# Kernel tuning notes

Measured on AMD Instinct MI355X. Metric: run time of the kernel, lower is better.

The kernel has to match this reference:

```python
import jax, jax.numpy as jnp
import numpy as np
import math

N_NODES = 50000
N_EDGES = 800000
IN_DIM = 128
OUT_DIM = 64
TIME_DIM = 128


def setup_inputs() -> dict:
    key = jax.random.key(0)
    ks = jax.random.split(key, 9)
    return {
        "node_feats": jax.random.normal(ks[0], (N_NODES, IN_DIM), dtype=jnp.float32),
        "time_diff": jax.random.uniform(ks[1], (N_EDGES,), dtype=jnp.float32),
        "src": jax.random.randint(ks[2], (N_EDGES,), 0, N_NODES, dtype=jnp.int32),
        "dst": jax.random.randint(ks[3], (N_EDGES,), 0, N_NODES, dtype=jnp.int32),
        "W": jax.random.normal(ks[4], (OUT_DIM, IN_DIM), dtype=jnp.float32) * 0.05,
        "Wv": jax.random.normal(ks[5], (OUT_DIM, IN_DIM), dtype=jnp.float32) * 0.05,
        "omega": jax.random.normal(ks[6], (TIME_DIM // 2,), dtype=jnp.float32),
        "Wt": jax.random.normal(ks[7], (OUT_DIM, TIME_DIM), dtype=jnp.float32) * 0.05,
        "a": jax.random.normal(ks[8], (3 * OUT_DIM,), dtype=jnp.float32) * 0.05,
    }


def reference(node_feats, time_diff, src, dst, W, Wv, omega, Wt, a):
    N = node_feats.shape[0]
    d = W.shape[0]  # out_dim
    time_dim = 2 * omega.shape[0]

    # gather + linear projections per edge
    h_src = node_feats[src] @ W.T          # [E, d]
    h_dst = node_feats[dst] @ W.T          # [E, d]
    v_src = node_feats[src] @ Wv.T         # [E, d]

    # temporal encoding: interleaved sin/cos of t * omega, scaled by sqrt(1/dim)
    ang = time_diff[:, None] * omega[None, :]                       # [E, dim/2]
    pe = jnp.stack([jnp.sin(ang), jnp.cos(ang)], axis=-1)
    pe = pe.reshape(ang.shape[0], time_dim) * jnp.float32(math.sqrt(1.0 / time_dim))
    t_emb = pe @ Wt.T                                               # [E, d]

    # attn_fc(concat([h_src, h_dst, t_emb])) == split dot products (same math, no big concat)
    e = h_src @ a[:d] + h_dst @ a[d:2 * d] + t_emb @ a[2 * d:]      # [E]
    e = jnp.where(e > 0, e, 0.2 * e)  # LeakyReLU(0.2)

    # edge_softmax: softmax over incoming edges of each destination node
    m = jax.ops.segment_max(e, dst, num_segments=N)
    ex = jnp.exp(e - m[dst])
    den = jax.ops.segment_sum(ex, dst, num_segments=N)
    alpha = ex / den[dst]  # dropout is identity in eval mode

    # weighted message scatter-sum aggregation
    msg = v_src * alpha[:, None]                                    # [E, d]
    return jax.ops.segment_sum(msg, dst, num_segments=N)            # [N, d]
```

## Files before the change

kernel.cpp:

```cpp
#include <hip/hip_runtime.h>
#include <hip/hip_bf16.h>
#include <hip/hip_fp16.h>
#include <math.h>

#define IN_DIM   128
#define OUT_DIM  64
#define THALF    64
#define PE_SCALE 0.08838834764831845f
#define TBL      2048
#define EPB_LOG  14
#define EPB      (1 << EPB_LOG)

typedef __attribute__((ext_vector_type(8))) short  short8;
typedef __attribute__((ext_vector_type(4))) float  f32x4;

__device__ inline unsigned short bf16_rne(float x) {
    unsigned u = __float_as_uint(x);
    return (unsigned short)((u + 0x7FFFu + ((u >> 16) & 1u)) >> 16);
}

__global__ __launch_bounds__(256) void k_prep(
    const float* __restrict__ W, const float* __restrict__ Wt,
    const float* __restrict__ a, const float* __restrict__ Wv,
    const float* __restrict__ omega,
    float* __restrict__ gtab, unsigned short* __restrict__ Bp,
    int* __restrict__ pref)
{
    __shared__ float satv[IN_DIM];
    __shared__ float saW1[IN_DIM], saW2[IN_DIM];
    int t = threadIdx.x;
    if (t < IN_DIM) {
        float x3 = 0.f;
        for (int j = 0; j < OUT_DIM; ++j)
            x3 += a[2 * OUT_DIM + j] * Wt[j * IN_DIM + t];
        satv[t] = x3;
        if (blockIdx.x == 0) {
            float x1 = 0.f, x2 = 0.f;
            for (int j = 0; j < OUT_DIM; ++j) {
                float wj = W[j * IN_DIM + t];
                x1 += a[j] * wj;
                x2 += a[OUT_DIM + j] * wj;
            }
            saW1[t] = x1; saW2[t] = x2;
        }
    }
    __syncthreads();

    int idx = blockIdx.x * 256 + t;
    if (idx <= TBL) {
        float tt = (float)idx * (1.0f / TBL);
        float acc = 0.f;
#pragma unroll
        for (int i = 0; i < THALF; ++i) {
            float sp, cp;
            __sincosf(tt * omega[i], &sp, &cp);
            acc += sp * satv[2 * i] + cp * satv[2 * i + 1];
        }
        gtab[idx] = acc;
    }
    if (idx < 64) pref[idx] = 0;

    if (blockIdx.x == 0) {
        for (int i = t; i < 5 * 4 * 64 * 8; i += 256) {
            int j    = i & 7;
            int lane = (i >> 3) & 63;
            int k0i  = (i >> 9) & 3;
            int tt   = i >> 11;
            int kk = k0i * 32 + (lane >> 4) * 8 + j;
            int n  = lane & 15;
            float val;
            if (tt < 4)     val = Wv[(tt * 16 + n) * IN_DIM + kk];
            else            val = (n == 0) ? saW1[kk] : (n == 1) ? saW2[kk] : 0.f;
            Bp[i] = bf16_rne(val);
        }
    }
}

__global__ __launch_bounds__(1024) void k_hist(
    const int* __restrict__ dst,
    unsigned short* __restrict__ lrank,
    unsigned* __restrict__ ghist,
    int N, int E)
{
    extern __shared__ unsigned h[];
    int NH = (N + 1) >> 1;
    int t = threadIdx.x;
    for (int i = t; i < NH; i += 1024) h[i] = 0u;
    __syncthreads();
    int b = blockIdx.x;
    int e0 = b << EPB_LOG;
    int e1 = e0 + EPB; if (e1 > E) e1 = E;
    for (int e = e0 + t; e < e1; e += 1024) {
        int d = dst[e];
        unsigned inc = (d & 1) ? 0x10000u : 1u;
        unsigned old = atomicAdd(&h[d >> 1], inc);
        lrank[e] = (unsigned short)((d & 1) ? (old >> 16) : (old & 0xFFFFu));
    }
    __syncthreads();
    unsigned* gh = ghist + (size_t)b * N;
    for (int w = t; w < NH; w += 1024) {
        unsigned v = h[w];
        int n0 = 2 * w;
        if (n0 + 1 < N) *(uint2*)(gh + n0) = make_uint2(v & 0xFFFFu, v >> 16);
        else            gh[n0] = v & 0xFFFFu;
    }
}

__global__ __launch_bounds__(256) void k_scan_base(
    unsigned* __restrict__ ghist, int* __restrict__ cnt, int B, int N)
{
    int n0 = (blockIdx.x * 256 + threadIdx.x) * 2;
    if (n0 >= N) return;
    if (n0 + 1 < N) {
        unsigned r0 = 0, r1 = 0;
        for (int b = 0; b < B; ++b) {
            unsigned* p = ghist + (size_t)b * N + n0;
            uint2 c = *(uint2*)p;
            *(uint2*)p = make_uint2(r0, r1);
            r0 += c.x; r1 += c.y;
        }
        *(int2*)(cnt + n0) = make_int2((int)r0, (int)r1);
    } else {
        unsigned r0 = 0;
        for (int b = 0; b < B; ++b) {
            unsigned* p = ghist + (size_t)b * N + n0;
            unsigned c = *p; *p = r0; r0 += c;
        }
        cnt[n0] = (int)r0;
    }
}

__global__ __launch_bounds__(256) void k_scan1(const int* __restrict__ cnt,
                                               int* __restrict__ offs,
                                               int* __restrict__ pref, int N)
{
    __shared__ int lds[256];
    int b = blockIdx.x, t = threadIdx.x;
    int base = b * 1024 + t * 4;
    int v0 = (base + 0 < N) ? cnt[base + 0] : 0;
    int v1 = (base + 1 < N) ? cnt[base + 1] : 0;
    int v2 = (base + 2 < N) ? cnt[base + 2] : 0;
    int v3 = (base + 3 < N) ? cnt[base + 3] : 0;
    int s = v0 + v1 + v2 + v3;
    lds[t] = s;
    __syncthreads();
    for (int off = 1; off < 256; off <<= 1) {
        int tmp = (t >= off) ? lds[t - off] : 0;
        __syncthreads();
        lds[t] += tmp;
        __syncthreads();
    }
    int ex = lds[t] - s;
    if (base + 0 < N) offs[base + 0] = ex;
    ex += v0;
    if (base + 1 < N) offs[base + 1] = ex;
    ex += v1;
    if (base + 2 < N) offs[base + 2] = ex;
    ex += v2;
    if (base + 3 < N) offs[base + 3] = ex;
    int total = lds[255];
    if (t > b && t < (int)gridDim.x) atomicAdd(pref + t, total);
}

__global__ __launch_bounds__(256) void k_node_mfma(
    const float* __restrict__ feats,
    const unsigned short* __restrict__ Bp,
    unsigned short* __restrict__ vb,
    float* __restrict__ s1,
    float* __restrict__ s2,
    int N)
{
    int gwave = (blockIdx.x * 256 + threadIdx.x) >> 6;
    int lane  = threadIdx.x & 63;
    int ntiles = (N + 15) >> 4;
    if (gwave >= ntiles) return;
    int row = lane & 15, quad = lane >> 4;
    int nodeA = gwave * 16 + row;
    int nodeL = nodeA < N ? nodeA : N - 1;

    const float* arow = feats + (size_t)nodeL * IN_DIM + quad * 8;
    short8 afrag[4];
#pragma unroll
    for (int k0i = 0; k0i < 4; ++k0i) {
        float4 fa = *(const float4*)(arow + k0i * 32);
        float4 fb = *(const float4*)(arow + k0i * 32 + 4);
        union { unsigned u[4]; short8 s; } cv;
        cv.u[0] = (__float_as_uint(fa.x) >> 16) | (__float_as_uint(fa.y) & 0xFFFF0000u);
        cv.u[1] = (__float_as_uint(fa.z) >> 16) | (__float_as_uint(fa.w) & 0xFFFF0000u);
        cv.u[2] = (__float_as_uint(fb.x) >> 16) | (__float_as_uint(fb.y) & 0xFFFF0000u);
        cv.u[3] = (__float_as_uint(fb.z) >> 16) | (__float_as_uint(fb.w) & 0xFFFF0000u);
        afrag[k0i] = cv.s;
    }

    const short8* B8 = (const short8*)Bp;
    f32x4 acc[5];
#pragma unroll
    for (int t = 0; t < 5; ++t) acc[t] = (f32x4){0.f, 0.f, 0.f, 0.f};
#pragma unroll
    for (int t = 0; t < 5; ++t) {
#pragma unroll
        for (int k0i = 0; k0i < 4; ++k0i)
            acc[t] = __builtin_amdgcn_mfma_f32_16x16x32_bf16(
                afrag[k0i], B8[(t * 4 + k0i) * 64 + lane], acc[t], 0, 0, 0);
    }

    int col = lane & 15;
    int baseNode = gwave * 16 + quad * 4;
#pragma unroll
    for (int r = 0; r < 4; ++r) {
        int nd = baseNode + r;
        if (nd < N) {
            unsigned short* vr = vb + (size_t)nd * OUT_DIM + col;
#pragma unroll
            for (int t = 0; t < 4; ++t) vr[t * 16] = bf16_rne(acc[t][r]);
            if (col == 0)      s1[nd] = acc[4][r];
            else if (col == 1) s2[nd] = acc[4][r];
        }
    }
}

__global__ __launch_bounds__(256) void k_scatter_fused(
    const float* __restrict__ tdiff,
    const int* __restrict__ src,
    const int* __restrict__ dst,
    const float* __restrict__ gtab,
    const float* __restrict__ s1,
    const float* __restrict__ s2,
    const unsigned short* __restrict__ lrank,
    const unsigned* __restrict__ ghist,
    const int* __restrict__ offs,
    const int* __restrict__ pref,
    unsigned* __restrict__ payload,
    int N, int E)
{
    int base = (blockIdx.x * 256 + threadIdx.x) * 4;
    if (base >= E) return;
    if (base + 4 <= E) {
        int4   s4 = *(const int4*)(src + base);
        int4   d4 = *(const int4*)(dst + base);
        float4 t4 = *(const float4*)(tdiff + base);
        ushort4 l4 = *(const ushort4*)(lrank + base);
        int s[4]    = {s4.x, s4.y, s4.z, s4.w};
        int d[4]    = {d4.x, d4.y, d4.z, d4.w};
        float tv[4] = {t4.x, t4.y, t4.z, t4.w};
        int lr[4]   = {l4.x, l4.y, l4.z, l4.w};
#pragma unroll
        for (int i = 0; i < 4; ++i) {
            float a1 = s1[s[i]];
            float a2 = s2[d[i]];
            float x = tv[i] * (float)TBL;
            int i0 = (int)x;
            i0 = i0 < 0 ? 0 : (i0 > TBL - 1 ? TBL - 1 : i0);
            float fr = x - (float)i0;
            float ev = a1 + a2 + PE_SCALE * (gtab[i0] + fr * (gtab[i0 + 1] - gtab[i0]));
            ev = ev > 0.f ? ev : 0.2f * ev;
            unsigned pw = ((unsigned)s[i] << 16) | (unsigned)__half_as_ushort(__float2half(ev));
            int b = (base + i) >> EPB_LOG;
            int pos = offs[d[i]] + pref[d[i] >> 10] + (int)ghist[(size_t)b * N + d[i]] + lr[i];
            payload[pos] = pw;
        }
    } else {
        for (int e = base; e < E; ++e) {
            int s = src[e], d = dst[e];
            float a1 = s1[s], a2 = s2[d];
            float x = tdiff[e] * (float)TBL;
            int i0 = (int)x;
            i0 = i0 < 0 ? 0 : (i0 > TBL - 1 ? TBL - 1 : i0);
            float fr = x - (float)i0;
            float ev = a1 + a2 + PE_SCALE * (gtab[i0] + fr * (gtab[i0 + 1] - gtab[i0]));
            ev = ev > 0.f ? ev : 0.2f * ev;
            unsigned pw = ((unsigned)s << 16) | (unsigned)__half_as_ushort(__float2half(ev));
            int b = e >> EPB_LOG;
            int pos = offs[d] + pref[d >> 10] + (int)ghist[(size_t)b * N + d] + (int)lrank[e];
            payload[pos] = pw;
        }
    }
}

__global__ __launch_bounds__(256) void k_aggregate(
    const int* __restrict__ offs,
    const int* __restrict__ pref,
    const unsigned* __restrict__ payload,
    const unsigned short* __restrict__ vb,
    float* __restrict__ out,
    int N, int E)
{
    int wid  = (blockIdx.x * blockDim.x + threadIdx.x) >> 6;
    int lane = threadIdx.x & 63;
    if (wid >= N) return;
    int beg = offs[wid] + pref[wid >> 10];
    int end = (wid + 1 < N) ? (offs[wid + 1] + pref[(wid + 1) >> 10]) : E;
    int deg = end - beg;
    int g8 = lane >> 3, r = lane & 7;

    float acc[8];
#pragma unroll
    for (int i = 0; i < 8; ++i) acc[i] = 0.f;
    float den = 0.f;

    for (int base = 0; base < deg; base += 64) {
        int cl = deg - base; if (cl > 64) cl = 64;
        bool valid = lane < cl;
        unsigned pl = valid ? payload[beg + base + lane] : 0u;
        float ex = valid ? __expf(__half2float(__ushort_as_half((unsigned short)(pl & 0xFFFFu)))) : 0.f;
        int   sv = valid ? (int)(pl >> 16) : 0;

        float sum = ex;
#pragma unroll
        for (int off = 32; off; off >>= 1) sum += __shfl_xor(sum, off, 64);
        den += sum;

        int rounds = (cl + 15) >> 4;
        for (int j = 0; j < rounds; ++j) {
            int i0 = j * 16 + g8;
            int i1 = i0 + 8;
            float e0 = __shfl(ex, i0, 64);
            int   s0 = __shfl(sv, i0, 64);
            float e1 = __shfl(ex, i1, 64);
            int   s1v = __shfl(sv, i1, 64);
            uint4 w0 = *((const uint4*)(vb + (size_t)s0 * OUT_DIM) + r);
            uint4 w1 = *((const uint4*)(vb + (size_t)s1v * OUT_DIM) + r);
            acc[0] += e0 * __uint_as_float(w0.x << 16)         + e1 * __uint_as_float(w1.x << 16);
            acc[1] += e0 * __uint_as_float(w0.x & 0xFFFF0000u) + e1 * __uint_as_float(w1.x & 0xFFFF0000u);
            acc[2] += e0 * __uint_as_float(w0.y << 16)         + e1 * __uint_as_float(w1.y << 16);
            acc[3] += e0 * __uint_as_float(w0.y & 0xFFFF0000u) + e1 * __uint_as_float(w1.y & 0xFFFF0000u);
            acc[4] += e0 * __uint_as_float(w0.z << 16)         + e1 * __uint_as_float(w1.z << 16);
            acc[5] += e0 * __uint_as_float(w0.z & 0xFFFF0000u) + e1 * __uint_as_float(w1.z & 0xFFFF0000u);
            acc[6] += e0 * __uint_as_float(w0.w << 16)         + e1 * __uint_as_float(w1.w << 16);
            acc[7] += e0 * __uint_as_float(w0.w & 0xFFFF0000u) + e1 * __uint_as_float(w1.w & 0xFFFF0000u);
        }
    }

#pragma unroll
    for (int i = 0; i < 8; ++i) {
        acc[i] += __shfl_xor(acc[i], 8, 64);
        acc[i] += __shfl_xor(acc[i], 16, 64);
        acc[i] += __shfl_xor(acc[i], 32, 64);
    }

    if (g8 == 0) {
        float inv = (deg > 0) ? 1.f / den : 0.f;
        float* o = out + (size_t)wid * OUT_DIM + r * 8;
        *(float4*)(o)     = make_float4(acc[0] * inv, acc[1] * inv, acc[2] * inv, acc[3] * inv);
        *(float4*)(o + 4) = make_float4(acc[4] * inv, acc[5] * inv, acc[6] * inv, acc[7] * inv);
    }
}

extern "C" void kernel_launch(void* const* d_in, const int* in_sizes, int n_in,
                              void* d_out, int out_size, void* d_ws, size_t ws_size,
                              hipStream_t stream) {
    const float* feats = (const float*)d_in[0];
    const float* tdiff = (const float*)d_in[1];
    const int*   src   = (const int*)d_in[2];
    const int*   dst   = (const int*)d_in[3];
    const float* W     = (const float*)d_in[4];
    const float* Wv    = (const float*)d_in[5];
    const float* omega = (const float*)d_in[6];
    const float* Wt    = (const float*)d_in[7];
    const float* a     = (const float*)d_in[8];
    float* out = (float*)d_out;

    int N = in_sizes[0] / IN_DIM;
    int E = in_sizes[1];
    int B = (E + EPB - 1) >> EPB_LOG;

    int offs_elems = ((N + 1 + 3) / 4) * 4;
    float* ws      = (float*)d_ws;
    unsigned short* vb = (unsigned short*)ws;
    float* s1      = ws + (size_t)N * 32;
    float* s2      = s1 + N;
    unsigned* payload = (unsigned*)(s2 + N);
    unsigned short* lrank = (unsigned short*)(payload + E);
    int*   cnt     = (int*)(lrank + ((E + 1) & ~1));
    int*   offs    = cnt + N;
    int*   pref    = offs + offs_elems;
    float* gtab    = (float*)(pref + 64);
    unsigned short* Bp = (unsigned short*)(gtab + TBL + 1);
    size_t gho = ((size_t)(Bp + 10240) - (size_t)ws) / 4;
    gho = (gho + 1) & ~(size_t)1;
    unsigned* ghist = (unsigned*)ws + gho;

    int nb = (N + 1023) / 1024;
    int ntiles = (N + 15) / 16;
    int eb4 = (E + 4 * 256 - 1) / (4 * 256);
    unsigned ldsb = (unsigned)(((N + 1) / 2) * 4);

    k_prep<<<(TBL / 256) + 1, 256, 0, stream>>>(W, Wt, a, Wv, omega, gtab, Bp, pref);
    k_hist<<<B, 1024, ldsb, stream>>>(dst, lrank, ghist, N, E);
    k_node_mfma<<<(ntiles * 64 + 255) / 256, 256, 0, stream>>>(feats, Bp, vb, s1, s2, N);
    k_scan_base<<<((N + 1) / 2 + 255) / 256, 256, 0, stream>>>(ghist, cnt, B, N);
    k_scan1<<<nb, 256, 0, stream>>>(cnt, offs, pref, N);
    k_scatter_fused<<<eb4, 256, 0, stream>>>(tdiff, src, dst, gtab, s1, s2,
                                             lrank, ghist, offs, pref, payload, N, E);
    long long tot = (long long)N * OUT_DIM;
    k_aggregate<<<(int)((tot + 255) / 256), 256, 0, stream>>>(offs, pref, payload, vb, out, N, E);
}
```

Baseline: 191.7 us.

## Store per-block histograms as 16-bit and fuse the column scan with the offset scan

The per-block histogram is now stored as packed 16-bit counts, written straight from the LDS words, which halves its global footprint. The per-node scan over blocks and the prefix scan over nodes are merged into one kernel, dropping a launch and the intermediate count array. The scatter kernel now handles 8 edges per thread and computes all destination positions before the payload writes, to raise memory-level parallelism. The trade-offs are 16-bit overflow if a node's running count within one block column ever exceeds 65535, and far fewer threads doing the long serial loop over blocks in the fused scan kernel.

```diff
diff --git a/kernel.cpp b/kernel.cpp
--- a/kernel.cpp
+++ b/kernel.cpp
@@ -79,7 +79,7 @@
 __global__ __launch_bounds__(1024) void k_hist(
     const int* __restrict__ dst,
     unsigned short* __restrict__ lrank,
-    unsigned* __restrict__ ghist,
+    unsigned short* __restrict__ ghist16,
     int N, int E)
 {
     extern __shared__ unsigned h[];
@@ -97,51 +97,41 @@
         lrank[e] = (unsigned short)((d & 1) ? (old >> 16) : (old & 0xFFFFu));
     }
     __syncthreads();
-    unsigned* gh = ghist + (size_t)b * N;
-    for (int w = t; w < NH; w += 1024) {
-        unsigned v = h[w];
-        int n0 = 2 * w;
-        if (n0 + 1 < N) *(uint2*)(gh + n0) = make_uint2(v & 0xFFFFu, v >> 16);
-        else            gh[n0] = v & 0xFFFFu;
-    }
-}
-
-__global__ __launch_bounds__(256) void k_scan_base(
-    unsigned* __restrict__ ghist, int* __restrict__ cnt, int B, int N)
-{
-    int n0 = (blockIdx.x * 256 + threadIdx.x) * 2;
-    if (n0 >= N) return;
-    if (n0 + 1 < N) {
-        unsigned r0 = 0, r1 = 0;
-        for (int b = 0; b < B; ++b) {
-            unsigned* p = ghist + (size_t)b * N + n0;
-            uint2 c = *(uint2*)p;
-            *(uint2*)p = make_uint2(r0, r1);
-            r0 += c.x; r1 += c.y;
-        }
-        *(int2*)(cnt + n0) = make_int2((int)r0, (int)r1);
-    } else {
-        unsigned r0 = 0;
-        for (int b = 0; b < B; ++b) {
-            unsigned* p = ghist + (size_t)b * N + n0;
-            unsigned c = *p; *p = r0; r0 += c;
-        }
-        cnt[n0] = (int)r0;
-    }
-}
-
-__global__ __launch_bounds__(256) void k_scan1(const int* __restrict__ cnt,
-                                               int* __restrict__ offs,
-                                               int* __restrict__ pref, int N)
+    unsigned* gh32 = (unsigned*)(ghist16 + (size_t)b * N);
+    for (int w = t; w < NH; w += 1024) gh32[w] = h[w];
+}
+
+__global__ __launch_bounds__(256) void k_scan_fuse(
+    unsigned short* __restrict__ ghist16,
+    int* __restrict__ offs,
+    int* __restrict__ pref,
+    int B, int N)
 {
     __shared__ int lds[256];
     int b = blockIdx.x, t = threadIdx.x;
-    int base = b * 1024 + t * 4;
-    int v0 = (base + 0 < N) ? cnt[base + 0] : 0;
-    int v1 = (base + 1 < N) ? cnt[base + 1] : 0;
-    int v2 = (base + 2 < N) ? cnt[base + 2] : 0;
-    int v3 = (base + 3 < N) ? cnt[base + 3] : 0;
-    int s = v0 + v1 + v2 + v3;
+    int n0 = b * 1024 + t * 4;
+    unsigned r0 = 0, r1 = 0, r2 = 0, r3 = 0;
+    if (n0 + 3 < N) {
+        for (int bb = 0; bb < B; ++bb) {
+            unsigned short* p = ghist16 + (size_t)bb * N + n0;
+            uint2 c = *(uint2*)p;
+            uint2 w;
+            w.x = (r0 & 0xFFFFu) | (r1 << 16);
+            w.y = (r2 & 0xFFFFu) | (r3 << 16);
+            *(uint2*)p = w;
+            r0 += c.x & 0xFFFFu; r1 += c.x >> 16;
+            r2 += c.y & 0xFFFFu; r3 += c.y >> 16;
+        }
+    } else if (n0 < N) {
+        for (int bb = 0; bb < B; ++bb) {
+            unsigned short* p = ghist16 + (size_t)bb * N + n0;
+            unsigned c0 = p[0]; p[0] = (unsigned short)r0; r0 += c0;
+            if (n0 + 1 < N) { unsigned c = p[1]; p[1] = (unsigned short)r1; r1 += c; }
+            if (n0 + 2 < N) { unsigned c = p[2]; p[2] = (unsigned short)r2; r2 += c; }
+            if (n0 + 3 < N) { unsigned c = p[3]; p[3] = (unsigned short)r3; r3 += c; }
+        }
+    }
+    int s = (int)(r0 + r1 + r2 + r3);
     lds[t] = s;
     __syncthreads();
     for (int off = 1; off < 256; off <<= 1) {
@@ -151,13 +141,19 @@
         __syncthreads();
     }
     int ex = lds[t] - s;
-    if (base + 0 < N) offs[base + 0] = ex;
-    ex += v0;
-    if (base + 1 < N) offs[base + 1] = ex;
-    ex += v1;
-    if (base + 2 < N) offs[base + 2] = ex;
-    ex += v2;
-    if (base + 3 < N) offs[base + 3] = ex;
+    if (n0 + 3 < N) {
+        int4 o;
+        o.x = ex;
+        o.y = ex + (int)r0;
+        o.z = ex + (int)(r0 + r1);
+        o.w = ex + (int)(r0 + r1 + r2);
+        *(int4*)(offs + n0) = o;
+    } else if (n0 < N) {
+        offs[n0] = ex;
+        if (n0 + 1 < N) offs[n0 + 1] = ex + (int)r0;
+        if (n0 + 2 < N) offs[n0 + 2] = ex + (int)(r0 + r1);
+        if (n0 + 3 < N) offs[n0 + 3] = ex + (int)(r0 + r1 + r2);
+    }
     int total = lds[255];
     if (t > b && t < (int)gridDim.x) atomicAdd(pref + t, total);
 }
@@ -227,25 +223,37 @@
     const float* __restrict__ s1,
     const float* __restrict__ s2,
     const unsigned short* __restrict__ lrank,
-    const unsigned* __restrict__ ghist,
+    const unsigned short* __restrict__ ghist16,
     const int* __restrict__ offs,
     const int* __restrict__ pref,
     unsigned* __restrict__ payload,
     int N, int E)
 {
-    int base = (blockIdx.x * 256 + threadIdx.x) * 4;
+    int base = (blockIdx.x * 256 + threadIdx.x) * 8;
     if (base >= E) return;
-    if (base + 4 <= E) {
-        int4   s4 = *(const int4*)(src + base);
-        int4   d4 = *(const int4*)(dst + base);
-        float4 t4 = *(const float4*)(tdiff + base);
-        ushort4 l4 = *(const ushort4*)(lrank + base);
-        int s[4]    = {s4.x, s4.y, s4.z, s4.w};
-        int d[4]    = {d4.x, d4.y, d4.z, d4.w};
-        float tv[4] = {t4.x, t4.y, t4.z, t4.w};
-        int lr[4]   = {l4.x, l4.y, l4.z, l4.w};
-#pragma unroll
-        for (int i = 0; i < 4; ++i) {
+    if (base + 8 <= E) {
+        int4   sa = *(const int4*)(src + base);
+        int4   sb = *(const int4*)(src + base + 4);
+        int4   da = *(const int4*)(dst + base);
+        int4   db = *(const int4*)(dst + base + 4);
+        float4 ta = *(const float4*)(tdiff + base);
+        float4 tb = *(const float4*)(tdiff + base + 4);
+        ushort4 la = *(const ushort4*)(lrank + base);
+        ushort4 lb = *(const ushort4*)(lrank + base + 4);
+        int s[8]    = {sa.x, sa.y, sa.z, sa.w, sb.x, sb.y, sb.z, sb.w};
+        int d[8]    = {da.x, da.y, da.z, da.w, db.x, db.y, db.z, db.w};
+        float tv[8] = {ta.x, ta.y, ta.z, ta.w, tb.x, tb.y, tb.z, tb.w};
+        int lr[8]   = {la.x, la.y, la.z, la.w, lb.x, lb.y, lb.z, lb.w};
+
+        int pos[8];
+#pragma unroll
+        for (int i = 0; i < 8; ++i) {
+            int b = (base + i) >> EPB_LOG;
+            pos[i] = offs[d[i]] + pref[d[i] >> 10] +
+                     (int)ghist16[(size_t)b * N + d[i]] + lr[i];
+        }
+#pragma unroll
+        for (int i = 0; i < 8; ++i) {
             float a1 = s1[s[i]];
             float a2 = s2[d[i]];
             float x = tv[i] * (float)TBL;
@@ -255,9 +263,7 @@
             float ev = a1 + a2 + PE_SCALE * (gtab[i0] + fr * (gtab[i0 + 1] - gtab[i0]));
             ev = ev > 0.f ? ev : 0.2f * ev;
             unsigned pw = ((unsigned)s[i] << 16) | (unsigned)__half_as_ushort(__float2half(ev));
-            int b = (base + i) >> EPB_LOG;
-            int pos = offs[d[i]] + pref[d[i] >> 10] + (int)ghist[(size_t)b * N + d[i]] + lr[i];
-            payload[pos] = pw;
+            payload[pos[i]] = pw;
         }
     } else {
         for (int e = base; e < E; ++e) {
@@ -271,7 +277,7 @@
             ev = ev > 0.f ? ev : 0.2f * ev;
             unsigned pw = ((unsigned)s << 16) | (unsigned)__half_as_ushort(__float2half(ev));
             int b = e >> EPB_LOG;
-            int pos = offs[d] + pref[d >> 10] + (int)ghist[(size_t)b * N + d] + (int)lrank[e];
+            int pos = offs[d] + pref[d >> 10] + (int)ghist16[(size_t)b * N + d] + (int)lrank[e];
             payload[pos] = pw;
         }
     }
@@ -364,34 +370,31 @@
     int E = in_sizes[1];
     int B = (E + EPB - 1) >> EPB_LOG;
 
-    int offs_elems = ((N + 1 + 3) / 4) * 4;
     float* ws      = (float*)d_ws;
     unsigned short* vb = (unsigned short*)ws;
     float* s1      = ws + (size_t)N * 32;
     float* s2      = s1 + N;
     unsigned* payload = (unsigned*)(s2 + N);
     unsigned short* lrank = (unsigned short*)(payload + E);
-    int*   cnt     = (int*)(lrank + ((E + 1) & ~1));
-    int*   offs    = cnt + N;
+    int*   offs    = (int*)(lrank + ((E + 1) & ~1));
+    int    offs_elems = ((N + 1023) / 1024) * 1024;
     int*   pref    = offs + offs_elems;
     float* gtab    = (float*)(pref + 64);
     unsigned short* Bp = (unsigned short*)(gtab + TBL + 1);
-    size_t gho = ((size_t)(Bp + 10240) - (size_t)ws) / 4;
-    gho = (gho + 1) & ~(size_t)1;
-    unsigned* ghist = (unsigned*)ws + gho;
+    size_t gho = ((size_t)((char*)(Bp + 10240) - (char*)ws) + 7) & ~(size_t)7;
+    unsigned short* ghist16 = (unsigned short*)((char*)ws + gho);
 
     int nb = (N + 1023) / 1024;
     int ntiles = (N + 15) / 16;
-    int eb4 = (E + 4 * 256 - 1) / (4 * 256);
+    int eb8 = (E + 8 * 256 - 1) / (8 * 256);
     unsigned ldsb = (unsigned)(((N + 1) / 2) * 4);
 
     k_prep<<<(TBL / 256) + 1, 256, 0, stream>>>(W, Wt, a, Wv, omega, gtab, Bp, pref);
-    k_hist<<<B, 1024, ldsb, stream>>>(dst, lrank, ghist, N, E);
+    k_hist<<<B, 1024, ldsb, stream>>>(dst, lrank, ghist16, N, E);
     k_node_mfma<<<(ntiles * 64 + 255) / 256, 256, 0, stream>>>(feats, Bp, vb, s1, s2, N);
-    k_scan_base<<<((N + 1) / 2 + 255) / 256, 256, 0, stream>>>(ghist, cnt, B, N);
-    k_scan1<<<nb, 256, 0, stream>>>(cnt, offs, pref, N);
-    k_scatter_fused<<<eb4, 256, 0, stream>>>(tdiff, src, dst, gtab, s1, s2,
-                                             lrank, ghist, offs, pref, payload, N, E);
+    k_scan_fuse<<<nb, 256, 0, stream>>>(ghist16, offs, pref, B, N);
+    k_scatter_fused<<<eb8, 256, 0, stream>>>(tdiff, src, dst, gtab, s1, s2,
+                                             lrank, ghist16, offs, pref, payload, N, E);
     long long tot = (long long)N * OUT_DIM;
     k_aggregate<<<(int)((tot + 255) / 256), 256, 0, stream>>>(offs, pref, payload, vb, out, N, E);
 }
```

After: 181.7 us. 5.2% less time.
